# Optimization experiments

Measured on AMD Instinct MI355X. Metric: run time of the kernel, lower is better.

Reference implementation:

```python
import jax, jax.numpy as jnp
from jax import lax
import numpy as np

B, T, E, H, DA, HEADS, V = 128, 512, 256, 256, 25, 5, 2080
NEG = -1e30


def setup_inputs() -> dict:
    key = jax.random.key(0)
    ks = jax.random.split(key, 10)
    word_ids = jax.random.randint(ks[0], (B, T), 0, V)
    lengths = jax.random.randint(ks[1], (B,), 1, T + 1)  # >=1, original skips empty captions
    emb = jax.random.normal(ks[2], (V, E), dtype=jnp.float32)  # normal_(0,1) init
    sc = 0.05
    W_ih_f = jax.random.normal(ks[3], (4 * H, E), dtype=jnp.float32) * sc
    W_hh_f = jax.random.normal(ks[4], (4 * H, H), dtype=jnp.float32) * sc
    W_ih_b = jax.random.normal(ks[5], (4 * H, E), dtype=jnp.float32) * sc
    W_hh_b = jax.random.normal(ks[6], (4 * H, H), dtype=jnp.float32) * sc
    b_f = jnp.zeros((4 * H,), jnp.float32)  # biases init constant 0
    b_b = jnp.zeros((4 * H,), jnp.float32)
    W_s1 = jax.random.normal(ks[7], (DA, 2 * H), dtype=jnp.float32) * sc
    W_s2 = jax.random.normal(ks[8], (HEADS, DA), dtype=jnp.float32) * sc
    return dict(word_ids=word_ids, lengths=lengths, emb=emb,
                W_ih_f=W_ih_f, W_hh_f=W_hh_f, b_f=b_f,
                W_ih_b=W_ih_b, W_hh_b=W_hh_b, b_b=b_b,
                W_s1=W_s1, W_s2=W_s2)


def _lstm(x, W_ih, W_hh, b):
    # x: [B,T,E] -> outputs [B,T,H]; PyTorch gate order i,f,g,o; zero init state
    px = jnp.einsum('bte,ge->tbg', x, W_ih) + b  # [T,B,4H], input proj precomputed
    h0 = jnp.zeros((x.shape[0], W_hh.shape[1]), x.dtype)

    def step(carry, p):
        h, c = carry
        g = p + h @ W_hh.T
        i, f, gg, o = jnp.split(g, 4, axis=-1)
        c = jax.nn.sigmoid(f) * c + jax.nn.sigmoid(i) * jnp.tanh(gg)
        h = jax.nn.sigmoid(o) * jnp.tanh(c)
        return (h, c), h

    _, hs = lax.scan(step, (h0, h0), px)
    return hs.transpose(1, 0, 2)  # [B,T,H]


def _forward(word_ids, lengths, emb, W_ih_f, W_hh_f, b_f, W_ih_b, W_hh_b, b_b, W_s1, W_s2):
    x = emb[word_ids]  # [B,T,E]
    tpos = jnp.arange(T)
    mask = tpos[None, :] < lengths[:, None]  # [B,T] valid positions
    # per-sample reversal within its own length (garbage tail comes after valid prefix)
    rev_idx = jnp.clip(lengths[:, None] - 1 - tpos[None, :], 0)  # [B,T]
    x_rev = jnp.take_along_axis(x, rev_idx[:, :, None], axis=1)
    h_fwd = _lstm(x, W_ih_f, W_hh_f, b_f)                       # [B,T,H]
    h_bwd_rev = _lstm(x_rev, W_ih_b, W_hh_b, b_b)
    h_bwd = jnp.take_along_axis(h_bwd_rev, rev_idx[:, :, None], axis=1)  # back to original order
    Hc = jnp.concatenate([h_fwd, h_bwd], axis=-1)               # [B,T,2H]
    # attention: softmax over time per head, masked to valid length
    s = jnp.tanh(Hc @ W_s1.T) @ W_s2.T                          # [B,T,heads]
    logits = jnp.where(mask[:, :, None], s, NEG)
    A = jax.nn.softmax(logits, axis=1).transpose(0, 2, 1)       # [B,heads,T]
    A = A * mask[:, None, :].astype(A.dtype)                    # exact zeros outside length
    M = jnp.einsum('bht,btd->bhd', A, Hc)                       # [B,heads,2H]
    sentence_embeddings = M.reshape(M.shape[0], -1)             # [B, heads*2H]
    AAt = jnp.einsum('bht,bgt->bhg', A, A)
    AAt = AAt * (1.0 - jnp.eye(HEADS, dtype=AAt.dtype))         # zero diagonal
    penal = jnp.sum(AAt * AAt) / M.shape[0]                     # mean of Frobenius^2
    return sentence_embeddings, penal


def reference(word_ids, lengths, emb, W_ih_f, W_hh_f, b_f, W_ih_b, W_hh_b, b_b, W_s1, W_s2):
    return _forward(word_ids, lengths, emb, W_ih_f, W_hh_f, b_f, W_ih_b, W_hh_b, b_b, W_s1, W_s2)
```

## Files before the change

kernel.cpp:

```cpp
#include <hip/hip_runtime.h>
#include <math.h>

#define T 512
#define B 128
#define E 256
#define H 256
#define G 1024
#define DA 25
#define HEADS 5
#define V 2080
#define NEGINF (-1e30f)

static constexpr size_t WBT_OFF  = 0;
static constexpr size_t WIH_OFF  = 1048576;
static constexpr size_t WS1M_OFF = 2097152;
static constexpr size_t PX_OFF   = 2148352;
static constexpr size_t HC_OFF   = 69257216;
static constexpr size_t HBUF_OFF = 203474944;
static constexpr size_t CST_OFF  = 203737088;
static constexpr size_t A_OFF    = 203999232;
static constexpr size_t PART_OFF = 205309952;
static constexpr size_t EMBH_OFF = 205310464;
static constexpr size_t EMBH_END = EMBH_OFF + (size_t)V * E * 2;
static constexpr size_t PM_OFF   = PX_OFF;
static constexpr size_t PP_OFF   = PX_OFF + 10485760;

static constexpr unsigned LSTM_LDS_BYTES = 160304;

typedef _Float16 half2v __attribute__((ext_vector_type(2)));
typedef _Float16 half8_ __attribute__((ext_vector_type(8)));
typedef float    f32x4  __attribute__((ext_vector_type(4)));

#if __has_builtin(__builtin_amdgcn_exp2f)
#define EXP2F_(x) __builtin_amdgcn_exp2f(x)
#else
#define EXP2F_(x) exp2f(x)
#endif
#if __has_builtin(__builtin_amdgcn_rcpf)
#define RCPF_(x) __builtin_amdgcn_rcpf(x)
#else
#define RCPF_(x) (1.0f / (x))
#endif

__device__ __forceinline__ float sigmoidf_(float x) { return 1.f / (1.f + expf(-x)); }

__device__ __forceinline__ float sigmoid_fast_(float x) {
    return RCPF_(1.f + EXP2F_(-1.44269504f * x));
}
__device__ __forceinline__ float tanh_fast_(float x) {
    return 1.f - 2.f * RCPF_(1.f + EXP2F_(2.88539008f * x));
}

__device__ __forceinline__ unsigned short f2h_(float f) {
    _Float16 h = (_Float16)f;
    unsigned short u;
    __builtin_memcpy(&u, &h, 2);
    return u;
}

__device__ __forceinline__ float fdot2_(unsigned w, half2v h, float acc) {
#if __has_builtin(__builtin_amdgcn_fdot2)
    half2v wv;
    __builtin_memcpy(&wv, &w, 4);
    return __builtin_amdgcn_fdot2(wv, h, acc, false);
#else
    unsigned short lo = (unsigned short)(w & 0xffffu), hi = (unsigned short)(w >> 16);
    _Float16 w0, w1;
    __builtin_memcpy(&w0, &lo, 2);
    __builtin_memcpy(&w1, &hi, 2);
    return fmaf((float)w0, (float)h[0], fmaf((float)w1, (float)h[1], acc));
#endif
}

__device__ __forceinline__ half2v packh2_(float a, float b) {
    half2v h;
    h[0] = (_Float16)a;
    h[1] = (_Float16)b;
    return h;
}

__global__ __launch_bounds__(256) void prep_kernel(const float* __restrict__ Whf,
                                                   const float* __restrict__ Whb,
                                                   const float* __restrict__ Wif,
                                                   const float* __restrict__ Wib,
                                                   const float* __restrict__ Ws1,
                                                   const float* __restrict__ emb,
                                                   unsigned short* __restrict__ wbt,
                                                   unsigned short* __restrict__ wih,
                                                   unsigned short* __restrict__ ws1m,
                                                   unsigned short* __restrict__ embh) {
    int idx = blockIdx.x * 256 + threadIdx.x;
    if (idx < 2 * G * H) {
        int d = idx >> 18;
        int rem = idx & 262143;
        int r = rem >> 8;
        int k = rem & 255;
        const float* W = d ? Whb : Whf;
        int gate = r >> 8, j = r & 255;
        int k2 = k >> 1, ke = k & 1;
        wbt[(((size_t)d * 128 + k2) * 256 + j) * 8 + gate * 2 + ke] = f2h_(W[(size_t)r * H + k]);
        const float* Wi = d ? Wib : Wif;
        wih[((size_t)d * G + r) * 256 + k] = f2h_(Wi[(size_t)r * E + k]);
    }
    if (idx < 32 * 512) {
        int r = idx >> 9, k = idx & 511;
        ws1m[idx] = (r < DA) ? f2h_(Ws1[r * 512 + k]) : (unsigned short)0;
    }
    if (embh && idx < V * E) embh[idx] = f2h_(emb[idx]);
}

__global__ __launch_bounds__(256) void proj_kernel(const int* __restrict__ word_ids,
                                                   const int* __restrict__ lengths,
                                                   const float* __restrict__ emb,
                                                   const unsigned* __restrict__ embh,
                                                   const unsigned* __restrict__ wih,
                                                   const float* __restrict__ bf,
                                                   const float* __restrict__ bb,
                                                   float* __restrict__ pxc, int chunk) {
    int g0 = blockIdx.x * 64;
    int b  = blockIdx.y;
    int d  = blockIdx.z;
    int len = lengths[b];
    int t0 = chunk * 64;
    if (t0 >= len) return;
    const float* bias = d ? bb : bf;

    __shared__ _Float16 A_s[64][264];
    __shared__ _Float16 B_s[64][264];

    int tid = threadIdx.x;
    int sr = tid >> 2, sq = tid & 3;

    {
        int t = t0 + sr;
        int src = d ? max(len - 1 - t, 0) : t;
        int wid = word_ids[b * T + src];
        if (embh) {
            const uint4* ap = (const uint4*)embh + (size_t)wid * 32;
            #pragma unroll
            for (int c = 0; c < 8; c++) {
                uint4 v = ap[sq * 8 + c];
                *(uint4*)&A_s[sr][(sq * 8 + c) * 8] = v;
            }
        } else {
            const float4* ep = (const float4*)(emb + (size_t)wid * E);
            #pragma unroll
            for (int c = 0; c < 8; c++) {
                float4 x0 = ep[(sq * 8 + c) * 2];
                float4 x1 = ep[(sq * 8 + c) * 2 + 1];
                half8_ hv;
                hv[0] = (_Float16)x0.x; hv[1] = (_Float16)x0.y;
                hv[2] = (_Float16)x0.z; hv[3] = (_Float16)x0.w;
                hv[4] = (_Float16)x1.x; hv[5] = (_Float16)x1.y;
                hv[6] = (_Float16)x1.z; hv[7] = (_Float16)x1.w;
                *(half8_*)&A_s[sr][(sq * 8 + c) * 8] = hv;
            }
        }
        const uint4* bp = (const uint4*)wih + ((size_t)d * G + g0 + sr) * 32;
        #pragma unroll
        for (int c = 0; c < 8; c++) {
            uint4 v = bp[sq * 8 + c];
            *(uint4*)&B_s[sr][(sq * 8 + c) * 8] = v;
        }
    }
    __syncthreads();

    int lane = tid & 63, wave = tid >> 6;
    int m0 = (wave >> 1) * 32;
    int n0 = (wave & 1) * 32;
    int lr = lane & 15, lq = lane >> 4;

    f32x4 acc00 = {0.f, 0.f, 0.f, 0.f}, acc01 = {0.f, 0.f, 0.f, 0.f};
    f32x4 acc10 = {0.f, 0.f, 0.f, 0.f}, acc11 = {0.f, 0.f, 0.f, 0.f};

    #pragma unroll
    for (int k0 = 0; k0 < E; k0 += 32) {
        int ka = k0 + lq * 8;
        half8_ af0 = *(const half8_*)&A_s[m0 + lr][ka];
        half8_ af1 = *(const half8_*)&A_s[m0 + 16 + lr][ka];
        half8_ bf0 = *(const half8_*)&B_s[n0 + lr][ka];
        half8_ bf1 = *(const half8_*)&B_s[n0 + 16 + lr][ka];
        acc00 = __builtin_amdgcn_mfma_f32_16x16x32_f16(af0, bf0, acc00, 0, 0, 0);
        acc01 = __builtin_amdgcn_mfma_f32_16x16x32_f16(af0, bf1, acc01, 0, 0, 0);
        acc10 = __builtin_amdgcn_mfma_f32_16x16x32_f16(af1, bf0, acc10, 0, 0, 0);
        acc11 = __builtin_amdgcn_mfma_f32_16x16x32_f16(af1, bf1, acc11, 0, 0, 0);
    }

    float bia0 = bias[g0 + n0 + lr];
    float bia1 = bias[g0 + n0 + 16 + lr];
    #pragma unroll
    for (int mi = 0; mi < 2; mi++) {
        f32x4 ar0 = mi ? acc10 : acc00;
        f32x4 ar1 = mi ? acc11 : acc01;
        #pragma unroll
        for (int rr = 0; rr < 4; rr++) {
            int s = m0 + mi * 16 + lq * 4 + rr;
            float* dst = pxc + ((size_t)(d * 64 + s) * B + b) * G + g0;
            dst[n0 + lr]      = ar0[rr] + bia0;
            dst[n0 + 16 + lr] = ar1[rr] + bia1;
        }
    }
}

__global__ __launch_bounds__(1024, 4) void lstm6_kernel(const int* __restrict__ lengths,
                                                        const unsigned* __restrict__ wbt,
                                                        const float* __restrict__ pxc,
                                                        float* __restrict__ hc_out,
                                                        float* __restrict__ hbuf,
                                                        float* __restrict__ cstate,
                                                        int chunk) {
    int b   = blockIdx.x;
    int d   = blockIdx.y;
    int tid = threadIdx.x;
    int j  = tid & 255;
    int kq = tid >> 8;

    int len = lengths[b];
    int t0 = chunk * 64;
    if (t0 >= len) return;
    int tend = min(t0 + 64, len);

    extern __shared__ char smem[];
    unsigned* hh   = (unsigned*)smem;
    float4*   part = (float4*)(smem + 512);
    uint4*    wst  = (uint4*)(smem + 12848);
    unsigned short* hh16 = (unsigned short*)smem;

    float* hbufg = hbuf + ((size_t)d * B + b) * 256;

    float c = 0.f, hreg = 0.f;
    if (chunk == 0) {
        if (tid < 128) hh[tid] = 0u;
    } else {
        if (kq == 0) c = cstate[((size_t)d * B + b) * H + j];
        if (tid < 128) {
            half2v hv2 = packh2_(hbufg[2 * tid], hbufg[2 * tid + 1]);
            unsigned hu;
            __builtin_memcpy(&hu, &hv2, 4);
            hh[tid] = hu;
        }
    }

    const uint4* wp  = (const uint4*)wbt + ((size_t)d * 128 + kq * 32) * 256 + j;
    const float* pxd = pxc + (size_t)d * 64 * B * G;

    #pragma unroll
    for (int r = 0; r < 9; r++)
        wst[(kq * 9 + r) * 256 + j] = wp[(size_t)r * 256];
    uint4 wr0  = wp[9 * 256],  wr1  = wp[10 * 256], wr2  = wp[11 * 256];
    uint4 wr3  = wp[12 * 256], wr4  = wp[13 * 256], wr5  = wp[14 * 256];
    uint4 wr6  = wp[15 * 256], wr7  = wp[16 * 256], wr8  = wp[17 * 256];
    uint4 wr9  = wp[18 * 256], wr10 = wp[19 * 256], wr11 = wp[20 * 256];
    uint4 wr12 = wp[21 * 256], wr13 = wp[22 * 256], wr14 = wp[23 * 256];
    __syncthreads();

    int hlane = kq * 32 + (tid & 31);
    int pendpos = -1;

    for (int t = t0; t < tend; t++) {
        int s = t - t0;

        if (kq == 0 && pendpos >= 0)
            hc_out[((size_t)b * T + pendpos) * (2 * H) + d * H + j] = hreg;

        float p0, p1, p2, p3;
        if (kq == 0) {
            const float* pxs = pxd + ((size_t)s * B + b) * G;
            p0 = pxs[j];
            p1 = pxs[256 + j];
            p2 = pxs[512 + j];
            p3 = pxs[768 + j];
        }

        unsigned hlv = hh[hlane];
        uint4 wv0 = wp[24 * 256], wv1 = wp[25 * 256], wv2 = wp[26 * 256], wv3 = wp[27 * 256];

        float a0 = 0.f, a1 = 0.f, a2 = 0.f, a3 = 0.f;

        #define HROW(IDX) __builtin_amdgcn_readlane(hlv, IDX)
        #define DOT4(WV, IDX)                                          \
            { unsigned hu = HROW(IDX); half2v hx;                      \
              __builtin_memcpy(&hx, &hu, 4);                           \
              a0 = fdot2_(WV.x, hx, a0); a1 = fdot2_(WV.y, hx, a1);    \
              a2 = fdot2_(WV.z, hx, a2); a3 = fdot2_(WV.w, hx, a3); }

        #pragma unroll
        for (int r = 0; r < 9; r++) {
            uint4 wv = wst[(kq * 9 + r) * 256 + j];
            DOT4(wv, r)
        }
        DOT4(wv0, 24) DOT4(wv1, 25) DOT4(wv2, 26) DOT4(wv3, 27)
        uint4 wv4 = wp[28 * 256], wv5 = wp[29 * 256], wv6 = wp[30 * 256], wv7 = wp[31 * 256];
        DOT4(wr0, 9)  DOT4(wr1, 10)  DOT4(wr2, 11)  DOT4(wr3, 12)
        DOT4(wr4, 13) DOT4(wr5, 14)  DOT4(wr6, 15)  DOT4(wr7, 16)
        DOT4(wr8, 17) DOT4(wr9, 18)  DOT4(wr10, 19) DOT4(wr11, 20)
        DOT4(wr12, 21) DOT4(wr13, 22) DOT4(wr14, 23)
        DOT4(wv4, 28) DOT4(wv5, 29) DOT4(wv6, 30) DOT4(wv7, 31)
        #undef DOT4
        #undef HROW

        if (kq > 0) part[(kq - 1) * 257 + j] = make_float4(a0, a1, a2, a3);
        __syncthreads();

        if (kq == 0) {
            __builtin_amdgcn_s_setprio(1);
            #pragma unroll
            for (int q = 0; q < 3; q++) {
                float4 qv = part[q * 257 + j];
                a0 += qv.x; a1 += qv.y; a2 += qv.z; a3 += qv.w;
            }
            a0 += p0; a1 += p1; a2 += p2; a3 += p3;

            float ig = sigmoid_fast_(a0), fg = sigmoid_fast_(a1), og = sigmoid_fast_(a3);
            c = fg * c + ig * tanh_fast_(a2);
            float h = og * tanh_fast_(c);
            hreg = h;
            hh16[j] = f2h_(h);
            pendpos = d ? (len - 1 - t) : t;
            __builtin_amdgcn_s_setprio(0);
        }
        __syncthreads();
    }

    if (kq == 0) {
        if (pendpos >= 0)
            hc_out[((size_t)b * T + pendpos) * (2 * H) + d * H + j] = hreg;
        cstate[((size_t)d * B + b) * H + j] = c;
        hbufg[j] = hreg;
    }
}

__global__ __launch_bounds__(256) void logits_kernel(const int* __restrict__ lengths,
                                                     const float* __restrict__ hc,
                                                     const uint4* __restrict__ ws1m,
                                                     const float* __restrict__ Ws2,
                                                     float* __restrict__ S) {
    __shared__ _Float16 A_s[64][520];
    __shared__ _Float16 B_s[32][520];

    int b = blockIdx.y, tt = blockIdx.x;
    int tid = threadIdx.x;
    int len = lengths[b];
    int t0 = tt * 64;

    int lane = tid & 63, wave = tid >> 6;
    int lr = lane & 15, lq = lane >> 4;
    int m0 = wave * 16;

    if (t0 >= len) {
        if (lr < HEADS) {
            #pragma unroll
            for (int rr = 0; rr < 4; rr++) {
                int t = t0 + m0 + lq * 4 + rr;
                S[((size_t)b * HEADS + lr) * T + t] = NEGINF;
            }
        }
        return;
    }

    {
        #pragma unroll
        for (int i = 0; i < 8; i++) {
            int u = tid + i * 256;
            int r = u >> 6, c8 = u & 63;
            *(uint4*)&B_s[r][c8 * 8] = ws1m[u];
        }
    }
    {
        int row = tid >> 2, q = tid & 3;
        int t = t0 + row;
        const float4* ep = (const float4*)(hc + ((size_t)b * T + t) * 512 + q * 128);
        #pragma unroll
        for (int c = 0; c < 16; c++) {
            float4 x0 = ep[2 * c];
            float4 x1 = ep[2 * c + 1];
            half8_ hv;
            hv[0] = (_Float16)x0.x; hv[1] = (_Float16)x0.y;
            hv[2] = (_Float16)x0.z; hv[3] = (_Float16)x0.w;
            hv[4] = (_Float16)x1.x; hv[5] = (_Float16)x1.y;
            hv[6] = (_Float16)x1.z; hv[7] = (_Float16)x1.w;
            *(half8_*)&A_s[row][q * 128 + c * 8] = hv;
        }
    }
    __syncthreads();

    f32x4 acc0 = {0.f, 0.f, 0.f, 0.f};
    f32x4 acc1 = {0.f, 0.f, 0.f, 0.f};
    #pragma unroll
    for (int ks = 0; ks < 16; ks++) {
        int ka = ks * 32 + lq * 8;
        half8_ af  = *(const half8_*)&A_s[m0 + lr][ka];
        half8_ bf0 = *(const half8_*)&B_s[lr][ka];
        half8_ bf1 = *(const half8_*)&B_s[16 + lr][ka];
        acc0 = __builtin_amdgcn_mfma_f32_16x16x32_f16(af, bf0, acc0, 0, 0, 0);
        acc1 = __builtin_amdgcn_mfma_f32_16x16x32_f16(af, bf1, acc1, 0, 0, 0);
    }

    float w2a[HEADS], w2b[HEADS];
    #pragma unroll
    for (int h = 0; h < HEADS; h++) {
        w2a[h] = Ws2[h * DA + lr];
        w2b[h] = (lr + 16 < DA) ? Ws2[h * DA + 16 + lr] : 0.f;
    }

    #pragma unroll
    for (int rr = 0; rr < 4; rr++) {
        float y0 = tanhf(acc0[rr]);
        float y1 = tanhf(acc1[rr]);
        int t = t0 + m0 + lq * 4 + rr;
        float sv[HEADS];
        #pragma unroll
        for (int h = 0; h < HEADS; h++) {
            float v = y0 * w2a[h] + y1 * w2b[h];
            v += __shfl_xor(v, 1, 16);
            v += __shfl_xor(v, 2, 16);
            v += __shfl_xor(v, 4, 16);
            v += __shfl_xor(v, 8, 16);
            sv[h] = v;
        }
        if (lr < HEADS) {
            S[((size_t)b * HEADS + lr) * T + t] = (t < len) ? sv[lr] : NEGINF;
        }
    }
}

__global__ __launch_bounds__(256) void softmax_kernel(float* __restrict__ S) {
    int row = blockIdx.x;
    float* p = S + (size_t)row * T;
    int tid = threadIdx.x;
    int lane = tid & 63, wave = tid >> 6;
    __shared__ float rr[4], ss[4];

    float mx = NEGINF;
    #pragma unroll
    for (int i = 0; i < 2; i++) mx = fmaxf(mx, p[tid + i * 256]);
    for (int off = 32; off; off >>= 1) mx = fmaxf(mx, __shfl_xor(mx, off, 64));
    if (lane == 0) rr[wave] = mx;
    __syncthreads();
    mx = fmaxf(fmaxf(rr[0], rr[1]), fmaxf(rr[2], rr[3]));

    float e[2], sum = 0.f;
    #pragma unroll
    for (int i = 0; i < 2; i++) { e[i] = expf(p[tid + i * 256] - mx); sum += e[i]; }
    for (int off = 32; off; off >>= 1) sum += __shfl_xor(sum, off, 64);
    if (lane == 0) ss[wave] = sum;
    __syncthreads();
    sum = ss[0] + ss[1] + ss[2] + ss[3];
    float inv = 1.f / sum;
    #pragma unroll
    for (int i = 0; i < 2; i++) p[tid + i * 256] = e[i] * inv;
}

__global__ __launch_bounds__(256) void attnM_part_kernel(const int* __restrict__ lengths,
                                                         const float* __restrict__ A,
                                                         const float* __restrict__ hc,
                                                         float* __restrict__ pm,
                                                         float* __restrict__ pp) {
    int tc = blockIdx.x, b = blockIdx.y, tid = threadIdx.x;
    int len = lengths[b];
    int t0 = tc * 64;
    int tend = min(t0 + 64, len);
    const float* Ab  = A + (size_t)b * HEADS * T;
    const float* hcb = hc + (size_t)b * T * (2 * H);
    float acc[HEADS][2];
    #pragma unroll
    for (int h = 0; h < HEADS; h++) { acc[h][0] = 0.f; acc[h][1] = 0.f; }
    float p[10];
    #pragma unroll
    for (int i = 0; i < 10; i++) p[i] = 0.f;

    for (int t = t0; t < tend; t++) {
        float v0 = hcb[(size_t)t * (2 * H) + tid];
        float v1 = hcb[(size_t)t * (2 * H) + H + tid];
        float a0 = Ab[t], a1 = Ab[T + t], a2 = Ab[2 * T + t], a3 = Ab[3 * T + t], a4 = Ab[4 * T + t];
        acc[0][0] += a0 * v0; acc[0][1] += a0 * v1;
        acc[1][0] += a1 * v0; acc[1][1] += a1 * v1;
        acc[2][0] += a2 * v0; acc[2][1] += a2 * v1;
        acc[3][0] += a3 * v0; acc[3][1] += a3 * v1;
        acc[4][0] += a4 * v0; acc[4][1] += a4 * v1;
        if ((t & 255) == tid) {
            p[0] += a0 * a1; p[1] += a0 * a2; p[2] += a0 * a3; p[3] += a0 * a4;
            p[4] += a1 * a2; p[5] += a1 * a3; p[6] += a1 * a4;
            p[7] += a2 * a3; p[8] += a2 * a4; p[9] += a3 * a4;
        }
    }
    size_t base = ((size_t)tc * B + b) * (HEADS * 2 * H);
    #pragma unroll
    for (int h = 0; h < HEADS; h++) {
        pm[base + h * (2 * H) + tid]     = acc[h][0];
        pm[base + h * (2 * H) + H + tid] = acc[h][1];
    }

    __shared__ float red[10][4];
    int lane = tid & 63, wave = tid >> 6;
    #pragma unroll
    for (int i = 0; i < 10; i++) {
        float v = p[i];
        for (int off = 32; off; off >>= 1) v += __shfl_xor(v, off, 64);
        if (lane == 0) red[i][wave] = v;
    }
    __syncthreads();
    if (tid < 10)
        pp[((size_t)tc * B + b) * 16 + tid] =
            red[tid][0] + red[tid][1] + red[tid][2] + red[tid][3];
}

__global__ __launch_bounds__(256) void attnM_reduce_kernel(const float* __restrict__ pm,
                                                           const float* __restrict__ pp,
                                                           float* __restrict__ out,
                                                           float* __restrict__ part) {
    int b = blockIdx.x, tid = threadIdx.x;
    #pragma unroll
    for (int h = 0; h < HEADS; h++) {
        float a0 = 0.f, a1 = 0.f;
        #pragma unroll
        for (int tc = 0; tc < 8; tc++) {
            size_t base = ((size_t)tc * B + b) * (HEADS * 2 * H) + h * (2 * H);
            a0 += pm[base + tid];
            a1 += pm[base + H + tid];
        }
        out[(size_t)b * (HEADS * 2 * H) + h * (2 * H) + tid]     = a0;
        out[(size_t)b * (HEADS * 2 * H) + h * (2 * H) + H + tid] = a1;
    }
    __shared__ float sred[10];
    if (tid < 10) {
        float P = 0.f;
        #pragma unroll
        for (int tc = 0; tc < 8; tc++) P += pp[((size_t)tc * B + b) * 16 + tid];
        sred[tid] = 2.f * P * P;
    }
    __syncthreads();
    if (tid == 0) {
        float s = 0.f;
        #pragma unroll
        for (int i = 0; i < 10; i++) s += sred[i];
        part[b] = s;
    }
}

__global__ __launch_bounds__(128) void final_kernel(const float* __restrict__ part,
                                                    float* __restrict__ out) {
    int tid = threadIdx.x;
    float v = part[tid];
    for (int off = 32; off; off >>= 1) v += __shfl_xor(v, off, 64);
    __shared__ float r2[2];
    if ((tid & 63) == 0) r2[tid >> 6] = v;
    __syncthreads();
    if (tid == 0) out[(size_t)B * HEADS * 2 * H] = (r2[0] + r2[1]) * (1.f / (float)B);
}

extern "C" void kernel_launch(void* const* d_in, const int* in_sizes, int n_in,
                              void* d_out, int out_size, void* d_ws, size_t ws_size,
                              hipStream_t stream) {
    const int*   word_ids = (const int*)d_in[0];
    const int*   lengths  = (const int*)d_in[1];
    const float* emb      = (const float*)d_in[2];
    const float* W_ih_f   = (const float*)d_in[3];
    const float* W_hh_f   = (const float*)d_in[4];
    const float* b_f      = (const float*)d_in[5];
    const float* W_ih_b   = (const float*)d_in[6];
    const float* W_hh_b   = (const float*)d_in[7];
    const float* b_b      = (const float*)d_in[8];
    const float* W_s1     = (const float*)d_in[9];
    const float* W_s2     = (const float*)d_in[10];
    float* out = (float*)d_out;

    char* ws = (char*)d_ws;
    unsigned short* wbt16 = (unsigned short*)(ws + WBT_OFF);
    unsigned*       wbt   = (unsigned*)(ws + WBT_OFF);
    unsigned short* wih16 = (unsigned short*)(ws + WIH_OFF);
    unsigned*       wihu  = (unsigned*)(ws + WIH_OFF);
    unsigned short* ws1m16 = (unsigned short*)(ws + WS1M_OFF);
    const uint4*    ws1m4  = (const uint4*)(ws + WS1M_OFF);
    float* pxc    = (float*)(ws + PX_OFF);
    float* hc     = (float*)(ws + HC_OFF);
    float* hbuf   = (float*)(ws + HBUF_OFF);
    float* cstate = (float*)(ws + CST_OFF);
    float* Abuf   = (float*)(ws + A_OFF);
    float* part   = (float*)(ws + PART_OFF);
    float* pm     = (float*)(ws + PM_OFF);
    float* pp     = (float*)(ws + PP_OFF);
    bool have_embh = (ws_size >= EMBH_END);
    unsigned short* embh16 = have_embh ? (unsigned short*)(ws + EMBH_OFF) : nullptr;
    const unsigned* embhu  = have_embh ? (const unsigned*)(ws + EMBH_OFF) : nullptr;

    prep_kernel<<<2080, 256, 0, stream>>>(W_hh_f, W_hh_b, W_ih_f, W_ih_b, W_s1, emb,
                                          wbt16, wih16, ws1m16, embh16);

    for (int c = 0; c < 8; c++) {
        proj_kernel<<<dim3(16, 128, 2), 256, 0, stream>>>(
            word_ids, lengths, emb, embhu, wihu, b_f, b_b, pxc, c);
        lstm6_kernel<<<dim3(128, 2), 1024, LSTM_LDS_BYTES, stream>>>(
            lengths, wbt, pxc, hc, hbuf, cstate, c);
    }

    logits_kernel<<<dim3(8, 128), 256, 0, stream>>>(lengths, hc, ws1m4, W_s2, Abuf);
    softmax_kernel<<<B * HEADS, 256, 0, stream>>>(Abuf);
    attnM_part_kernel<<<dim3(8, 128), 256, 0, stream>>>(lengths, Abuf, hc, pm, pp);
    attnM_reduce_kernel<<<B, 256, 0, stream>>>(pm, pp, out, part);
    final_kernel<<<1, 128, 0, stream>>>(part, out);
}
```

Measured before the change: 1.209 ms.

## Distribute LSTM gate math across all waves and pass h via shuffles

Every thread now reads the reduced partial sums from a double-buffered LDS array and recomputes the gate nonlinearities for its own hidden index. The new h is then packed to half2 and redistributed within each wave via shuffles, so the per-step h buffer in LDS and the second __syncthreads are both removed. The weights kept in LDS drop from 9 rows to 7, with more rows streamed from global memory each step, which shrinks the LDS footprint. The cost is that gate math and px loads are duplicated across the four k-groups, and more global weight traffic is issued per timestep.

After: 1.420 ms. 1.17x slower.

```diff
diff --git a/kernel.cpp b/kernel.cpp
--- a/kernel.cpp
+++ b/kernel.cpp
@@ -25,7 +25,7 @@
 static constexpr size_t PM_OFF   = PX_OFF;
 static constexpr size_t PP_OFF   = PX_OFF + 10485760;
 
-static constexpr unsigned LSTM_LDS_BYTES = 160304;
+static constexpr unsigned LSTM_LDS_BYTES = 147584;
 
 typedef _Float16 half2v __attribute__((ext_vector_type(2)));
 typedef _Float16 half8_ __attribute__((ext_vector_type(8)));
@@ -209,11 +209,14 @@
                                                         float* __restrict__ hbuf,
                                                         float* __restrict__ cstate,
                                                         int chunk) {
-    int b   = blockIdx.x;
-    int d   = blockIdx.y;
-    int tid = threadIdx.x;
-    int j  = tid & 255;
-    int kq = tid >> 8;
+    int b    = blockIdx.x;
+    int d    = blockIdx.y;
+    int tid  = threadIdx.x;
+    int j    = tid & 255;
+    int kq   = tid >> 8;
+    int lane = tid & 63;
+    int wave = tid >> 6;
+    int jf   = kq * 64 + lane;
 
     int len = lengths[b];
     int t0 = chunk * 64;
@@ -221,59 +224,44 @@
     int tend = min(t0 + 64, len);
 
     extern __shared__ char smem[];
-    unsigned* hh   = (unsigned*)smem;
-    float4*   part = (float4*)(smem + 512);
-    uint4*    wst  = (uint4*)(smem + 12848);
-    unsigned short* hh16 = (unsigned short*)smem;
+    float4* part = (float4*)smem;
+    uint4*  wst  = (uint4*)(smem + 32896);
 
     float* hbufg = hbuf + ((size_t)d * B + b) * 256;
 
     float c = 0.f, hreg = 0.f;
-    if (chunk == 0) {
-        if (tid < 128) hh[tid] = 0u;
-    } else {
-        if (kq == 0) c = cstate[((size_t)d * B + b) * H + j];
-        if (tid < 128) {
-            half2v hv2 = packh2_(hbufg[2 * tid], hbufg[2 * tid + 1]);
-            unsigned hu;
-            __builtin_memcpy(&hu, &hv2, 4);
-            hh[tid] = hu;
-        }
+    unsigned hlv = 0u;
+    if (chunk != 0) {
+        c = cstate[((size_t)d * B + b) * H + jf];
+        int m2 = kq * 64 + 2 * (lane & 31);
+        half2v hv2 = packh2_(hbufg[m2], hbufg[m2 + 1]);
+        __builtin_memcpy(&hlv, &hv2, 4);
+        hreg = hbufg[jf];
     }
 
     const uint4* wp  = (const uint4*)wbt + ((size_t)d * 128 + kq * 32) * 256 + j;
     const float* pxd = pxc + (size_t)d * 64 * B * G;
 
     #pragma unroll
-    for (int r = 0; r < 9; r++)
-        wst[(kq * 9 + r) * 256 + j] = wp[(size_t)r * 256];
-    uint4 wr0  = wp[9 * 256],  wr1  = wp[10 * 256], wr2  = wp[11 * 256];
-    uint4 wr3  = wp[12 * 256], wr4  = wp[13 * 256], wr5  = wp[14 * 256];
-    uint4 wr6  = wp[15 * 256], wr7  = wp[16 * 256], wr8  = wp[17 * 256];
-    uint4 wr9  = wp[18 * 256], wr10 = wp[19 * 256], wr11 = wp[20 * 256];
-    uint4 wr12 = wp[21 * 256], wr13 = wp[22 * 256], wr14 = wp[23 * 256];
-    __syncthreads();
-
-    int hlane = kq * 32 + (tid & 31);
-    int pendpos = -1;
+    for (int r = 0; r < 7; r++)
+        wst[(kq * 7 + r) * 256 + j] = wp[(size_t)r * 256];
+    uint4 wr0  = wp[7 * 256],  wr1  = wp[8 * 256],  wr2  = wp[9 * 256];
+    uint4 wr3  = wp[10 * 256], wr4  = wp[11 * 256], wr5  = wp[12 * 256];
+    uint4 wr6  = wp[13 * 256], wr7  = wp[14 * 256], wr8  = wp[15 * 256];
+    uint4 wr9  = wp[16 * 256], wr10 = wp[17 * 256], wr11 = wp[18 * 256];
+    uint4 wr12 = wp[19 * 256], wr13 = wp[20 * 256], wr14 = wp[21 * 256];
 
     for (int t = t0; t < tend; t++) {
         int s = t - t0;
 
-        if (kq == 0 && pendpos >= 0)
-            hc_out[((size_t)b * T + pendpos) * (2 * H) + d * H + j] = hreg;
-
-        float p0, p1, p2, p3;
-        if (kq == 0) {
-            const float* pxs = pxd + ((size_t)s * B + b) * G;
-            p0 = pxs[j];
-            p1 = pxs[256 + j];
-            p2 = pxs[512 + j];
-            p3 = pxs[768 + j];
-        }
-
-        unsigned hlv = hh[hlane];
-        uint4 wv0 = wp[24 * 256], wv1 = wp[25 * 256], wv2 = wp[26 * 256], wv3 = wp[27 * 256];
+        const float* pxs = pxd + ((size_t)s * B + b) * G;
+        float p0 = pxs[jf];
+        float p1 = pxs[256 + jf];
+        float p2 = pxs[512 + jf];
+        float p3 = pxs[768 + jf];
+
+        uint4 v22 = wp[22 * 256], v23 = wp[23 * 256], v24 = wp[24 * 256];
+        uint4 v25 = wp[25 * 256], v26 = wp[26 * 256];
 
         float a0 = 0.f, a1 = 0.f, a2 = 0.f, a3 = 0.f;
 
@@ -285,48 +273,54 @@
               a2 = fdot2_(WV.z, hx, a2); a3 = fdot2_(WV.w, hx, a3); }
 
         #pragma unroll
-        for (int r = 0; r < 9; r++) {
-            uint4 wv = wst[(kq * 9 + r) * 256 + j];
+        for (int r = 0; r < 7; r++) {
+            uint4 wv = wst[(kq * 7 + r) * 256 + j];
             DOT4(wv, r)
         }
-        DOT4(wv0, 24) DOT4(wv1, 25) DOT4(wv2, 26) DOT4(wv3, 27)
-        uint4 wv4 = wp[28 * 256], wv5 = wp[29 * 256], wv6 = wp[30 * 256], wv7 = wp[31 * 256];
-        DOT4(wr0, 9)  DOT4(wr1, 10)  DOT4(wr2, 11)  DOT4(wr3, 12)
-        DOT4(wr4, 13) DOT4(wr5, 14)  DOT4(wr6, 15)  DOT4(wr7, 16)
-        DOT4(wr8, 17) DOT4(wr9, 18)  DOT4(wr10, 19) DOT4(wr11, 20)
-        DOT4(wr12, 21) DOT4(wr13, 22) DOT4(wr14, 23)
-        DOT4(wv4, 28) DOT4(wv5, 29) DOT4(wv6, 30) DOT4(wv7, 31)
+        DOT4(v22, 22) DOT4(v23, 23) DOT4(v24, 24) DOT4(v25, 25) DOT4(v26, 26)
+        uint4 v27 = wp[27 * 256], v28 = wp[28 * 256], v29 = wp[29 * 256];
+        uint4 v30 = wp[30 * 256], v31 = wp[31 * 256];
+        DOT4(wr0, 7)   DOT4(wr1, 8)   DOT4(wr2, 9)   DOT4(wr3, 10)
+        DOT4(wr4, 11)  DOT4(wr5, 12)  DOT4(wr6, 13)  DOT4(wr7, 14)
+        DOT4(wr8, 15)  DOT4(wr9, 16)  DOT4(wr10, 17) DOT4(wr11, 18)
+        DOT4(wr12, 19) DOT4(wr13, 20) DOT4(wr14, 21)
+        DOT4(v27, 27) DOT4(v28, 28) DOT4(v29, 29) DOT4(v30, 30) DOT4(v31, 31)
         #undef DOT4
         #undef HROW
 
-        if (kq > 0) part[(kq - 1) * 257 + j] = make_float4(a0, a1, a2, a3);
+        part[((size_t)(t & 1) * 4 + kq) * 257 + j] = make_float4(a0, a1, a2, a3);
         __syncthreads();
 
-        if (kq == 0) {
-            __builtin_amdgcn_s_setprio(1);
-            #pragma unroll
-            for (int q = 0; q < 3; q++) {
-                float4 qv = part[q * 257 + j];
-                a0 += qv.x; a1 += qv.y; a2 += qv.z; a3 += qv.w;
-            }
-            a0 += p0; a1 += p1; a2 += p2; a3 += p3;
-
-            float ig = sigmoid_fast_(a0), fg = sigmoid_fast_(a1), og = sigmoid_fast_(a3);
-            c = fg * c + ig * tanh_fast_(a2);
-            float h = og * tanh_fast_(c);
-            hreg = h;
-            hh16[j] = f2h_(h);
-            pendpos = d ? (len - 1 - t) : t;
-            __builtin_amdgcn_s_setprio(0);
-        }
-        __syncthreads();
-    }
-
-    if (kq == 0) {
-        if (pendpos >= 0)
-            hc_out[((size_t)b * T + pendpos) * (2 * H) + d * H + j] = hreg;
-        cstate[((size_t)d * B + b) * H + j] = c;
-        hbufg[j] = hreg;
+        const float4* pb = part + (size_t)(t & 1) * 4 * 257;
+        float4 q0 = pb[0 * 257 + jf];
+        float4 q1 = pb[1 * 257 + jf];
+        float4 q2 = pb[2 * 257 + jf];
+        float4 q3 = pb[3 * 257 + jf];
+        float f0 = ((q0.x + q1.x) + (q2.x + q3.x)) + p0;
+        float f1 = ((q0.y + q1.y) + (q2.y + q3.y)) + p1;
+        float f2 = ((q0.z + q1.z) + (q2.z + q3.z)) + p2;
+        float f3 = ((q0.w + q1.w) + (q2.w + q3.w)) + p3;
+
+        float ig = sigmoid_fast_(f0), fg = sigmoid_fast_(f1), og = sigmoid_fast_(f3);
+        c = fg * c + ig * tanh_fast_(f2);
+        float h = og * tanh_fast_(c);
+        hreg = h;
+
+        if ((wave & 3) == 0) {
+            int pos = d ? (len - 1 - t) : t;
+            hc_out[((size_t)b * T + pos) * (2 * H) + d * H + jf] = h;
+        }
+
+        float hn = __shfl_down(h, 1);
+        half2v pr = packh2_(h, hn);
+        unsigned u;
+        __builtin_memcpy(&u, &pr, 4);
+        hlv = __shfl(u, 2 * (lane & 31), 64);
+    }
+
+    if ((wave & 3) == 0) {
+        cstate[((size_t)d * B + b) * H + jf] = c;
+        hbufg[jf] = hreg;
     }
 }
 
```
